# Kernel tuning notes

Measured on AMD Instinct MI355X. Metric: run time of the kernel, lower is better.

Reference implementation:

```python
import jax, jax.numpy as jnp
import numpy as np
from jax import lax

LRELU_SLOPE = 0.2
EPS = 1e-8


def eq_linear(x, W, b):
    # EqualizedLinear: weight scaled by 1/sqrt(fan_in)
    c = 1.0 / np.sqrt(W.shape[1])
    return x @ (W * c).T + b


def mod_conv(x, s, W, demod):
    # x: [b, cin, h, w], s: [b, cin], W: [cout, cin, k, k]
    b, cin, h, w = x.shape
    cout, _, k, _ = W.shape
    c = 1.0 / np.sqrt(cin * k * k)
    weights = (W * c)[None] * s[:, None, :, None, None]  # [b, cout, cin, k, k]
    if demod:
        sigma_inv = lax.rsqrt(jnp.sum(weights ** 2, axis=(2, 3, 4)) + EPS)  # [b, cout]
        weights = weights * sigma_inv[:, :, None, None, None]
    x2 = x.reshape(1, b * cin, h, w)
    wk = weights.reshape(b * cout, cin, k, k)
    pad = k // 2
    out = lax.conv_general_dilated(
        x2, wk, window_strides=(1, 1), padding=[(pad, pad), (pad, pad)],
        dimension_numbers=("NCHW", "OIHW", "NCHW"), feature_group_count=b)
    return out.reshape(b, cout, h, w)


def style_block(x, w, noise, style_W, style_b, conv_W, scale_noise, bias):
    A = eq_linear(w, style_W, style_b)          # [b, cin]
    x = mod_conv(x, A, conv_W, demod=True)      # [b, cout, h, w]
    if noise is not None:
        x = x + scale_noise[None, :, None, None] * noise
    return jax.nn.leaky_relu(x + bias[None, :, None, None], LRELU_SLOPE)


def rgb_block(x, w, style_W, style_b, conv_W, bias):
    A = eq_linear(w, style_W, style_b)
    x = mod_conv(x, A, conv_W, demod=False)     # 1x1 conv to 3 channels
    return jax.nn.leaky_relu(x + bias[None, :, None, None], LRELU_SLOPE)


def setup_inputs() -> dict:
    key = jax.random.key(0)
    ks = jax.random.split(key, 10)
    B, CIN, COUT, WD, H, W = 8, 512, 512, 512, 64, 64
    return {
        "x": jax.random.normal(ks[0], (B, CIN, H, W), jnp.float32),
        "w": jax.random.normal(ks[1], (B, WD), jnp.float32),
        "noise": jax.random.normal(ks[2], (2, B, 1, H, W), jnp.float32),
        # StyleBlock 1
        "s1_style_W": jax.random.normal(ks[3], (CIN, WD), jnp.float32),
        "s1_style_b": jnp.ones((CIN,), jnp.float32),
        "s1_conv_W": jax.random.normal(ks[4], (COUT, CIN, 3, 3), jnp.float32),
        "s1_scale_noise": jnp.zeros((1,), jnp.float32),
        "s1_bias": jnp.zeros((COUT,), jnp.float32),
        # StyleBlock 2
        "s2_style_W": jax.random.normal(ks[5], (COUT, WD), jnp.float32),
        "s2_style_b": jnp.ones((COUT,), jnp.float32),
        "s2_conv_W": jax.random.normal(ks[6], (COUT, COUT, 3, 3), jnp.float32),
        "s2_scale_noise": jnp.zeros((1,), jnp.float32),
        "s2_bias": jnp.zeros((COUT,), jnp.float32),
        # RGBBlock
        "rgb_style_W": jax.random.normal(ks[7], (COUT, WD), jnp.float32),
        "rgb_style_b": jnp.ones((COUT,), jnp.float32),
        "rgb_conv_W": jax.random.normal(ks[8], (3, COUT, 1, 1), jnp.float32),
        "rgb_bias": jnp.zeros((3,), jnp.float32),
    }


def reference(x, w, noise,
              s1_style_W, s1_style_b, s1_conv_W, s1_scale_noise, s1_bias,
              s2_style_W, s2_style_b, s2_conv_W, s2_scale_noise, s2_bias,
              rgb_style_W, rgb_style_b, rgb_conv_W, rgb_bias):
    x = style_block(x, w, noise[0], s1_style_W, s1_style_b, s1_conv_W, s1_scale_noise, s1_bias)
    x = style_block(x, w, noise[1], s2_style_W, s2_style_b, s2_conv_W, s2_scale_noise, s2_bias)
    rgb = rgb_block(x, w, rgb_style_W, rgb_style_b, rgb_conv_W, rgb_bias)
    return (x, rgb)
```

## Files before the change

kernel.cpp:

```cpp
#include <hip/hip_runtime.h>
#include <stdint.h>

typedef __attribute__((ext_vector_type(8))) short bf16x8;
typedef __attribute__((ext_vector_type(4))) float f32x4;

__device__ __forceinline__ ushort f2bf(float f) {
  uint32_t u = __builtin_bit_cast(uint32_t, f);
  u += 0x7fffu + ((u >> 16) & 1u);
  return (ushort)(u >> 16);
}

__device__ __forceinline__ void async_copy16(const void* gsrc, void* ldst) {
  __builtin_amdgcn_global_load_lds(
      (const __attribute__((address_space(1))) void*)gsrc,
      (__attribute__((address_space(3))) void*)ldst, 16, 0, 0);
}

__global__ void style_linear(const float* __restrict__ w, const float* __restrict__ sW,
                             const float* __restrict__ sb, float* __restrict__ A) {
  const int b = blockIdx.y;
  const int lane = threadIdx.x & 63, wv = threadIdx.x >> 6;
  const int co = blockIdx.x * 4 + wv;
  const float c = 0.04419417382415922f;
  const float* wr = w + b * 512;
  const float* Wr = sW + (size_t)co * 512;
  float s = 0.f;
#pragma unroll
  for (int i = 0; i < 8; ++i) {
    const int d = i * 64 + lane;
    s += wr[d] * Wr[d];
  }
#pragma unroll
  for (int off = 32; off; off >>= 1) s += __shfl_xor(s, off);
  if (lane == 0) A[b * 512 + co] = s * c + sb[co];
}

__global__ void prep_sigma(const float* __restrict__ Wc, const float* __restrict__ A,
                           ushort* __restrict__ Wt, float* __restrict__ sig) {
  const int co = blockIdx.x;
  const int ci = threadIdx.x;
  const int lane = ci & 63, wid = ci >> 6;
  const float c = 0.014731391274719738f;
  const float* src = Wc + ((size_t)co * 512 + ci) * 9;
  float s = 0.f;
#pragma unroll
  for (int t = 0; t < 9; ++t) {
    float v = src[t] * c;
    Wt[(size_t)t * 262144 + co * 512 + ci] = f2bf(v);
    s += v * v;
  }
  __shared__ float red[8][8];
#pragma unroll
  for (int b = 0; b < 8; ++b) {
    float a = A[b * 512 + ci];
    float v = s * a * a;
#pragma unroll
    for (int off = 32; off; off >>= 1) v += __shfl_xor(v, off);
    if (lane == 0) red[b][wid] = v;
  }
  __syncthreads();
  if (ci < 8) {
    float t = 0.f;
#pragma unroll
    for (int wv = 0; wv < 8; ++wv) t += red[ci][wv];
    sig[ci * 512 + co] = rsqrtf(t + 1e-8f);
  }
}

__global__ void zero_border(uint4* __restrict__ x1, uint4* __restrict__ x2) {
  const int i = blockIdx.x * 256 + threadIdx.x;
  const int per = 16640;
  const int tot = per * 8;
  if (i >= 2 * tot) return;
  uint4* base = (i < tot) ? x1 : x2;
  int t = (i < tot) ? i : i - tot;
  const int bb = t / per;
  int r = t - bb * per;
  int row, cell, q;
  if (r < 8448) {
    row = (r >= 4224) ? 65 : 0;
    int pos = (r >= 4224) ? r - 4224 : r;
    cell = pos >> 6;
    q = pos & 63;
  } else {
    int r2 = r - 8448;
    row = 1 + (r2 >> 7);
    cell = ((r2 >> 6) & 1) ? 65 : 0;
    q = r2 & 63;
  }
  base[(((size_t)bb * 66 + row) * 66 + cell) * 64 + q] = make_uint4(0u, 0u, 0u, 0u);
}

__global__ void mod_transpose(const float* __restrict__ X, const float* __restrict__ A,
                              ushort* __restrict__ xs) {
  __shared__ float tile[128][65];
  const int h = blockIdx.x;
  const int ci0 = blockIdx.y * 128;
  const int b = blockIdx.z;
  const int tid = threadIdx.x;
  const int wcol = tid & 63;
  const int r0 = tid >> 6;
#pragma unroll 4
  for (int i = 0; i < 32; ++i) {
    const int cil = r0 + i * 4;
    const int ci = ci0 + cil;
    const size_t off = ((size_t)(b * 512 + ci) * 64 + h) * 64 + wcol;
    tile[cil][wcol] = X[off] * A[b * 512 + ci];
  }
  __syncthreads();
  const int sub = tid & 3;
  const int w = tid >> 2;
  ushort* dst = xs + (((size_t)b * 66 + (h + 1)) * 66 + (w + 1)) * 512 + ci0 + sub * 32;
#pragma unroll
  for (int g = 0; g < 4; ++g) {
    bf16x8 v;
#pragma unroll
    for (int j = 0; j < 8; ++j) v[j] = (short)f2bf(tile[sub * 32 + g * 8 + j][w]);
    *(bf16x8*)(dst + g * 8) = v;
  }
}

#define WAITVM(N) asm volatile("s_waitcnt vmcnt(" #N ")" ::: "memory")

#define PHASE(S, WN, DOSTAGE)                                                        \
  do {                                                                               \
    WAITVM(WN);                                                                      \
    asm volatile("" ::: "memory");                                                   \
    __builtin_amdgcn_s_barrier();                                                    \
    asm volatile("" ::: "memory");                                                   \
    const int q_ = (S) & 3;                                                          \
    const char* baA = (const char*)(&smA[0][0] + q_ * 8192);                         \
    const char* baB = (const char*)(&smB[0][0] + q_ * 8192);                         \
    bf16x8 af[8], bv[4];                                                             \
    _Pragma("unroll") for (int m_ = 0; m_ < 8; ++m_)                                 \
        af[m_] = *(const bf16x8*)(baA + aro[m_]);                                    \
    _Pragma("unroll") for (int n_ = 0; n_ < 4; ++n_)                                 \
        bv[n_] = *(const bf16x8*)(baB + bro[n_]);                                    \
    if (DOSTAGE) stage((S) + 3);                                                     \
    __builtin_amdgcn_sched_barrier(0);                                               \
    __builtin_amdgcn_s_setprio(1);                                                   \
    _Pragma("unroll") for (int m_ = 0; m_ < 8; ++m_)                                 \
      _Pragma("unroll") for (int n_ = 0; n_ < 4; ++n_)                               \
        acc[m_][n_] = __builtin_amdgcn_mfma_f32_16x16x32_bf16(af[m_], bv[n_],        \
                                                              acc[m_][n_], 0, 0, 0); \
    __builtin_amdgcn_s_setprio(0);                                                   \
    __builtin_amdgcn_sched_barrier(0);                                               \
  } while (0)

template <int OUT_MODE>
__global__ __launch_bounds__(512, 2) void conv3x3(
    const ushort* __restrict__ xs, const ushort* __restrict__ Wt,
    const float* __restrict__ sig, const float* __restrict__ noise,
    const float* __restrict__ scale_noise, const float* __restrict__ bias,
    const float* __restrict__ amod, void* __restrict__ outp) {
  __shared__ __align__(16) ushort smA[4][8192];
  __shared__ __align__(16) ushort smB[4][8192];
  const int tid = threadIdx.x, lane = tid & 63, wid = tid >> 6;
  const int wr = wid >> 2, wc = wid & 3;
  const int id = blockIdx.x;
  const int b = id & 7;
  const int tile = id >> 3;
  const int co0 = (tile & 1) * 256;
  const int px0 = (tile >> 1) * 256;
  const int h0 = px0 >> 6;

  const int sswz = ((lane & 3) ^ ((lane >> 3) & 3)) * 8;
  int aoff[2], boff[2];
  ushort *ldsA[2], *ldsB[2];
#pragma unroll
  for (int i = 0; i < 2; ++i) {
    const int row = (i * 8 + wid) * 16 + (lane >> 2);
    aoff[i] = (co0 + row) * 512 + sswz;
    const int hh = h0 + (row >> 6), ww = row & 63;
    boff[i] = ((b * 66 + hh) * 66 + ww) * 512 + sswz;
    ldsA[i] = &smA[0][0] + (i * 8 + wid) * 512 + lane * 8;
    ldsB[i] = &smB[0][0] + (i * 8 + wid) * 512 + lane * 8;
  }
  const int rdsw = ((lane >> 4) ^ ((lane >> 1) & 3)) * 16;
  int aro[8], bro[4];
#pragma unroll
  for (int m = 0; m < 8; ++m) aro[m] = (wr * 128 + m * 16 + (lane & 15)) * 64 + rdsw;
#pragma unroll
  for (int n = 0; n < 4; ++n) bro[n] = (wc * 64 + n * 16 + (lane & 15)) * 64 + rdsw;

  f32x4 acc[8][4];
#pragma unroll
  for (int m = 0; m < 8; ++m)
#pragma unroll
    for (int n = 0; n < 4; ++n) acc[m][n] = (f32x4){0.f, 0.f, 0.f, 0.f};

  auto stage = [&](int s) {
    const int tap = s >> 4;
    const int ci0 = (s & 15) << 5;
    const int kh = tap / 3;
    const int kw = tap - kh * 3;
    const int q = s & 3;
    const ushort* Wb = Wt + tap * 262144 + ci0;
    const ushort* Xb = xs + (kh * 66 + kw) * 512 + ci0;
    async_copy16(Wb + aoff[0], ldsA[0] + q * 8192);
    async_copy16(Wb + aoff[1], ldsA[1] + q * 8192);
    async_copy16(Xb + boff[0], ldsB[0] + q * 8192);
    async_copy16(Xb + boff[1], ldsB[1] + q * 8192);
  };

  stage(0);
  stage(1);
  stage(2);

  for (int s = 0; s < 140; s += 4) {
    PHASE(s + 0, 8, true);
    PHASE(s + 1, 8, true);
    PHASE(s + 2, 8, true);
    PHASE(s + 3, 8, true);
  }
  PHASE(140, 8, true);
  PHASE(141, 8, false);
  PHASE(142, 4, false);
  PHASE(143, 0, false);

  const float sn = scale_noise[0];
  const int colp = lane & 15;
  const int rq = (lane >> 4) * 4;
  float nz[4];
#pragma unroll
  for (int n = 0; n < 4; ++n)
    nz[n] = sn * noise[b * 4096 + px0 + wc * 64 + n * 16 + colp];
#pragma unroll
  for (int m = 0; m < 8; ++m) {
    const int cob = co0 + wr * 128 + m * 16 + rq;
    float sg[4], bs[4], am[4];
#pragma unroll
    for (int r = 0; r < 4; ++r) {
      sg[r] = sig[b * 512 + cob + r];
      bs[r] = bias[cob + r];
      am[r] = (OUT_MODE == 0) ? amod[b * 512 + cob + r] : 0.f;
    }
#pragma unroll
    for (int n = 0; n < 4; ++n) {
      const int px = px0 + wc * 64 + n * 16 + colp;
      if (OUT_MODE == 0) {
        const int hh = px >> 6, ww = px & 63;
        ushort pk[4];
#pragma unroll
        for (int r = 0; r < 4; ++r) {
          float v = acc[m][n][r] * sg[r] + nz[n] + bs[r];
          v = (v > 0.f) ? v : 0.2f * v;
          pk[r] = f2bf(v * am[r]);
        }
        uint2 u;
        u.x = (uint32_t)pk[0] | ((uint32_t)pk[1] << 16);
        u.y = (uint32_t)pk[2] | ((uint32_t)pk[3] << 16);
        *(uint2*)((ushort*)outp + (((size_t)b * 66 + hh + 1) * 66 + (ww + 1)) * 512 + cob) = u;
      } else {
#pragma unroll
        for (int r = 0; r < 4; ++r) {
          float v = acc[m][n][r] * sg[r] + nz[n] + bs[r];
          v = (v > 0.f) ? v : 0.2f * v;
          ((float*)outp)[((size_t)b * 512 + cob + r) * 4096 + px] = v;
        }
      }
    }
  }
}

__global__ void rgb_k(const float* __restrict__ X, const float* __restrict__ Ar,
                      const float* __restrict__ rgbW, const float* __restrict__ rgbB,
                      float* __restrict__ out) {
  __shared__ float wmod[3 * 512];
  const int b = blockIdx.y;
  const int tid = threadIdx.x;
  const float c = 0.04419417382415922f;
  for (int idx = tid; idx < 1536; idx += 256)
    wmod[idx] = rgbW[idx] * c * Ar[b * 512 + (idx & 511)];
  __syncthreads();
  const int p = blockIdx.x * 256 + tid;
  const float* xb = X + (size_t)b * 512 * 4096 + p;
  float a0 = 0.f, a1 = 0.f, a2 = 0.f;
  for (int ci = 0; ci < 512; ++ci) {
    float xv = xb[(size_t)ci * 4096];
    a0 += wmod[ci] * xv;
    a1 += wmod[512 + ci] * xv;
    a2 += wmod[1024 + ci] * xv;
  }
  float v0 = a0 + rgbB[0], v1 = a1 + rgbB[1], v2 = a2 + rgbB[2];
  v0 = (v0 > 0.f) ? v0 : 0.2f * v0;
  v1 = (v1 > 0.f) ? v1 : 0.2f * v1;
  v2 = (v2 > 0.f) ? v2 : 0.2f * v2;
  out[((size_t)b * 3 + 0) * 4096 + p] = v0;
  out[((size_t)b * 3 + 1) * 4096 + p] = v1;
  out[((size_t)b * 3 + 2) * 4096 + p] = v2;
}

extern "C" void kernel_launch(void* const* d_in, const int* in_sizes, int n_in,
                              void* d_out, int out_size, void* d_ws, size_t ws_size,
                              hipStream_t stream) {
  const float* x     = (const float*)d_in[0];
  const float* w     = (const float*)d_in[1];
  const float* noise = (const float*)d_in[2];
  const float* s1_sW = (const float*)d_in[3];
  const float* s1_sb = (const float*)d_in[4];
  const float* s1_cW = (const float*)d_in[5];
  const float* s1_sn = (const float*)d_in[6];
  const float* s1_b  = (const float*)d_in[7];
  const float* s2_sW = (const float*)d_in[8];
  const float* s2_sb = (const float*)d_in[9];
  const float* s2_cW = (const float*)d_in[10];
  const float* s2_sn = (const float*)d_in[11];
  const float* s2_b  = (const float*)d_in[12];
  const float* r_sW  = (const float*)d_in[13];
  const float* r_sb  = (const float*)d_in[14];
  const float* r_cW  = (const float*)d_in[15];
  const float* r_b   = (const float*)d_in[16];

  char* ws = (char*)d_ws;
  float*  A1  = (float*)(ws + 0);
  float*  A2  = (float*)(ws + 16384);
  float*  Arr = (float*)(ws + 32768);
  float*  sg1 = (float*)(ws + 49152);
  float*  sg2 = (float*)(ws + 65536);
  ushort* Wt1 = (ushort*)(ws + 98304);
  ushort* xs1 = (ushort*)(ws + 4816896);
  ushort* Wt2 = (ushort*)(ws + 4816896);
  ushort* xs2 = (ushort*)(ws + 40501248);
  float* outx   = (float*)d_out;
  float* outrgb = outx + (size_t)8 * 512 * 4096;

  style_linear<<<dim3(128, 8), 256, 0, stream>>>(w, s1_sW, s1_sb, A1);
  style_linear<<<dim3(128, 8), 256, 0, stream>>>(w, s2_sW, s2_sb, A2);
  style_linear<<<dim3(128, 8), 256, 0, stream>>>(w, r_sW, r_sb, Arr);

  prep_sigma<<<512, 512, 0, stream>>>(s1_cW, A1, Wt1, sg1);

  zero_border<<<1040, 256, 0, stream>>>((uint4*)xs1, (uint4*)xs2);
  mod_transpose<<<dim3(64, 4, 8), 256, 0, stream>>>(x, A1, xs1);

  conv3x3<0><<<dim3(256), 512, 0, stream>>>(xs1, Wt1, sg1, noise, s1_sn, s1_b, A2, (void*)xs2);
  prep_sigma<<<512, 512, 0, stream>>>(s2_cW, A2, Wt2, sg2);
  conv3x3<1><<<dim3(256), 512, 0, stream>>>(xs2, Wt2, sg2, noise + 32768, s2_sn, s2_b, sg2,
                                            (void*)outx);
  rgb_k<<<dim3(16, 8), 256, 0, stream>>>(outx, Arr, r_cW, r_b, outrgb);
}
```

Baseline: 351.1 us.

## Split conv3x3 main loop into half-phases overlapping LDS reads with MFMAs

Restructures the K-loop of the conv3x3 GEMM into two sub-phases per stage. The upper half of the A fragments is read from LDS while MFMAs on the lower half run, and the next stage's lower-A and B fragments are prefetched while the upper-half MFMAs run, using double-buffered register fragments. The aim is to hide LDS read latency behind matrix-core work instead of waiting on all fragment loads before each MFMA batch. The vmcnt wait thresholds are also changed. The extra fragment registers add pressure at 512 threads with 2 blocks per CU, and the reworked barrier and wait placement risks LDS buffer races.

After: 360.5 us. +2.7%, slower.

```diff
diff --git a/kernel.cpp b/kernel.cpp
--- a/kernel.cpp
+++ b/kernel.cpp
@@ -122,29 +122,40 @@
 
 #define WAITVM(N) asm volatile("s_waitcnt vmcnt(" #N ")" ::: "memory")
 
-#define PHASE(S, WN, DOSTAGE)                                                        \
-  do {                                                                               \
-    WAITVM(WN);                                                                      \
-    asm volatile("" ::: "memory");                                                   \
-    __builtin_amdgcn_s_barrier();                                                    \
-    asm volatile("" ::: "memory");                                                   \
-    const int q_ = (S) & 3;                                                          \
-    const char* baA = (const char*)(&smA[0][0] + q_ * 8192);                         \
-    const char* baB = (const char*)(&smB[0][0] + q_ * 8192);                         \
-    bf16x8 af[8], bv[4];                                                             \
-    _Pragma("unroll") for (int m_ = 0; m_ < 8; ++m_)                                 \
-        af[m_] = *(const bf16x8*)(baA + aro[m_]);                                    \
-    _Pragma("unroll") for (int n_ = 0; n_ < 4; ++n_)                                 \
-        bv[n_] = *(const bf16x8*)(baB + bro[n_]);                                    \
-    if (DOSTAGE) stage((S) + 3);                                                     \
-    __builtin_amdgcn_sched_barrier(0);                                               \
-    __builtin_amdgcn_s_setprio(1);                                                   \
-    _Pragma("unroll") for (int m_ = 0; m_ < 8; ++m_)                                 \
-      _Pragma("unroll") for (int n_ = 0; n_ < 4; ++n_)                               \
-        acc[m_][n_] = __builtin_amdgcn_mfma_f32_16x16x32_bf16(af[m_], bv[n_],        \
-                                                              acc[m_][n_], 0, 0, 0); \
-    __builtin_amdgcn_s_setprio(0);                                                   \
-    __builtin_amdgcn_sched_barrier(0);                                               \
+#define MFMA_BF16(a, bb, c) __builtin_amdgcn_mfma_f32_16x16x32_bf16(a, bb, c, 0, 0, 0)
+
+#define SPA(S, AFL, BVC)                                                     \
+  do {                                                                       \
+    const char* baC = (const char*)(&smA[0][0]) + ((S) & 3) * 16384;         \
+    _Pragma("unroll") for (int m_ = 0; m_ < 4; ++m_)                         \
+        afH[m_] = *(const bf16x8*)(baC + aro[4 + m_]);                       \
+    __builtin_amdgcn_sched_barrier(0);                                       \
+    __builtin_amdgcn_s_setprio(1);                                           \
+    _Pragma("unroll") for (int m_ = 0; m_ < 4; ++m_)                         \
+      _Pragma("unroll") for (int n_ = 0; n_ < 4; ++n_)                       \
+          acc[m_][n_] = MFMA_BF16(AFL[m_], BVC[n_], acc[m_][n_]);            \
+    __builtin_amdgcn_s_setprio(0);                                           \
+    __builtin_amdgcn_sched_barrier(0);                                       \
+  } while (0)
+
+#define SPB(S, WN, DOSTAGE, AFLN, BVN, BVC)                                  \
+  do {                                                                       \
+    WAITVM(WN);                                                              \
+    __builtin_amdgcn_s_barrier();                                            \
+    const char* baA = (const char*)(&smA[0][0]) + (((S) + 1) & 3) * 16384;   \
+    const char* baB = (const char*)(&smB[0][0]) + (((S) + 1) & 3) * 16384;   \
+    _Pragma("unroll") for (int m_ = 0; m_ < 4; ++m_)                         \
+        AFLN[m_] = *(const bf16x8*)(baA + aro[m_]);                          \
+    _Pragma("unroll") for (int n_ = 0; n_ < 4; ++n_)                         \
+        BVN[n_] = *(const bf16x8*)(baB + bro[n_]);                           \
+    if (DOSTAGE) stage((S) + 3);                                             \
+    __builtin_amdgcn_sched_barrier(0);                                       \
+    __builtin_amdgcn_s_setprio(1);                                           \
+    _Pragma("unroll") for (int m_ = 0; m_ < 4; ++m_)                         \
+      _Pragma("unroll") for (int n_ = 0; n_ < 4; ++n_)                       \
+          acc[4 + m_][n_] = MFMA_BF16(afH[m_], BVC[n_], acc[4 + m_][n_]);    \
+    __builtin_amdgcn_s_setprio(0);                                           \
+    __builtin_amdgcn_sched_barrier(0);                                       \
   } while (0)
 
 template <int OUT_MODE>
@@ -203,20 +214,38 @@
     async_copy16(Xb + boff[1], ldsB[1] + q * 8192);
   };
 
+  bf16x8 afL0[4], afL1[4], bv0[4], bv1[4], afH[4];
+
   stage(0);
   stage(1);
   stage(2);
-
-  for (int s = 0; s < 140; s += 4) {
-    PHASE(s + 0, 8, true);
-    PHASE(s + 1, 8, true);
-    PHASE(s + 2, 8, true);
-    PHASE(s + 3, 8, true);
-  }
-  PHASE(140, 8, true);
-  PHASE(141, 8, false);
-  PHASE(142, 4, false);
-  PHASE(143, 0, false);
+  WAITVM(8);
+  __builtin_amdgcn_s_barrier();
+  {
+    const char* baA = (const char*)(&smA[0][0]);
+    const char* baB = (const char*)(&smB[0][0]);
+#pragma unroll
+    for (int m_ = 0; m_ < 4; ++m_) afL0[m_] = *(const bf16x8*)(baA + aro[m_]);
+#pragma unroll
+    for (int n_ = 0; n_ < 4; ++n_) bv0[n_] = *(const bf16x8*)(baB + bro[n_]);
+  }
+
+  for (int s = 0; s < 142; s += 2) {
+    SPA(s, afL0, bv0);
+    SPB(s, 4, (s + 3 <= 143), afL1, bv1, bv0);
+    SPA(s + 1, afL1, bv1);
+    SPB(s + 1, 4, (s + 4 <= 143), afL0, bv0, bv1);
+  }
+  SPA(142, afL0, bv0);
+  SPB(142, 0, false, afL1, bv1, bv0);
+  SPA(143, afL1, bv1);
+  __builtin_amdgcn_s_setprio(1);
+#pragma unroll
+  for (int m_ = 0; m_ < 4; ++m_)
+#pragma unroll
+    for (int n_ = 0; n_ < 4; ++n_)
+      acc[4 + m_][n_] = MFMA_BF16(afH[m_], bv1[n_], acc[4 + m_][n_]);
+  __builtin_amdgcn_s_setprio(0);
 
   const float sn = scale_noise[0];
   const int colp = lane & 15;
```

## Halve conv pixel tile and use triple-buffered LDS for higher occupancy

Applied to the files above, without the earlier changes.

The implicit-GEMM conv tile changes from 256x256 to 256 cout by 128 pixels, and each wave now computes a 64x64 sub-tile with half as many accumulators. The LDS ring drops from four stages to three, and the launch bound rises to four blocks per CU, while the grid doubles to 512 blocks. The aim is to fill all CUs and raise occupancy so latency is hidden by more resident waves. In exchange, weights are reloaded more often, data reuse per MFMA falls, and the prefetch distance is shorter.

Result: slower. 390.8 us (+11.3%).

```diff
diff --git a/kernel.cpp b/kernel.cpp
--- a/kernel.cpp
+++ b/kernel.cpp
@@ -122,24 +122,23 @@
 
 #define WAITVM(N) asm volatile("s_waitcnt vmcnt(" #N ")" ::: "memory")
 
-#define PHASE(S, WN, DOSTAGE)                                                        \
+#define PHASE(S, Q, QS, WN, DOSTAGE)                                                 \
   do {                                                                               \
     WAITVM(WN);                                                                      \
     asm volatile("" ::: "memory");                                                   \
     __builtin_amdgcn_s_barrier();                                                    \
     asm volatile("" ::: "memory");                                                   \
-    const int q_ = (S) & 3;                                                          \
-    const char* baA = (const char*)(&smA[0][0] + q_ * 8192);                         \
-    const char* baB = (const char*)(&smB[0][0] + q_ * 8192);                         \
-    bf16x8 af[8], bv[4];                                                             \
-    _Pragma("unroll") for (int m_ = 0; m_ < 8; ++m_)                                 \
+    const char* baA = (const char*)(&smA[0][0]) + (Q) * 16384;                       \
+    const char* baB = (const char*)(&smB[0][0]) + (Q) * 8192;                        \
+    bf16x8 af[4], bv[4];                                                             \
+    _Pragma("unroll") for (int m_ = 0; m_ < 4; ++m_)                                 \
         af[m_] = *(const bf16x8*)(baA + aro[m_]);                                    \
     _Pragma("unroll") for (int n_ = 0; n_ < 4; ++n_)                                 \
         bv[n_] = *(const bf16x8*)(baB + bro[n_]);                                    \
-    if (DOSTAGE) stage((S) + 3);                                                     \
+    if (DOSTAGE) stage((S) + 2, (QS));                                               \
     __builtin_amdgcn_sched_barrier(0);                                               \
     __builtin_amdgcn_s_setprio(1);                                                   \
-    _Pragma("unroll") for (int m_ = 0; m_ < 8; ++m_)                                 \
+    _Pragma("unroll") for (int m_ = 0; m_ < 4; ++m_)                                 \
       _Pragma("unroll") for (int n_ = 0; n_ < 4; ++n_)                               \
         acc[m_][n_] = __builtin_amdgcn_mfma_f32_16x16x32_bf16(af[m_], bv[n_],        \
                                                               acc[m_][n_], 0, 0, 0); \
@@ -148,75 +147,73 @@
   } while (0)
 
 template <int OUT_MODE>
-__global__ __launch_bounds__(512, 2) void conv3x3(
+__global__ __launch_bounds__(512, 4) void conv3x3(
     const ushort* __restrict__ xs, const ushort* __restrict__ Wt,
     const float* __restrict__ sig, const float* __restrict__ noise,
     const float* __restrict__ scale_noise, const float* __restrict__ bias,
     const float* __restrict__ amod, void* __restrict__ outp) {
-  __shared__ __align__(16) ushort smA[4][8192];
-  __shared__ __align__(16) ushort smB[4][8192];
-  const int tid = threadIdx.x, lane = tid & 63, wid = tid >> 6;
-  const int wr = wid >> 2, wc = wid & 3;
+  __shared__ __align__(16) ushort smA[3][8192];
+  __shared__ __align__(16) ushort smB[3][4096];
+  const int tid = threadIdx.x, lane = tid & 63;
+  const int wid = tid >> 6;
+  const int wr = wid >> 1, wc = wid & 1;
   const int id = blockIdx.x;
   const int b = id & 7;
   const int tile = id >> 3;
   const int co0 = (tile & 1) * 256;
-  const int px0 = (tile >> 1) * 256;
+  const int px0 = (tile >> 1) * 128;
   const int h0 = px0 >> 6;
 
   const int sswz = ((lane & 3) ^ ((lane >> 3) & 3)) * 8;
-  int aoff[2], boff[2];
-  ushort *ldsA[2], *ldsB[2];
-#pragma unroll
-  for (int i = 0; i < 2; ++i) {
-    const int row = (i * 8 + wid) * 16 + (lane >> 2);
-    aoff[i] = (co0 + row) * 512 + sswz;
-    const int hh = h0 + (row >> 6), ww = row & 63;
-    boff[i] = ((b * 66 + hh) * 66 + ww) * 512 + sswz;
-    ldsA[i] = &smA[0][0] + (i * 8 + wid) * 512 + lane * 8;
-    ldsB[i] = &smB[0][0] + (i * 8 + wid) * 512 + lane * 8;
-  }
+  int aoff[2], boff;
+  {
+    const int rowA0 = tid >> 2;
+    aoff[0] = (co0 + rowA0) * 512 + sswz;
+    aoff[1] = (co0 + 128 + rowA0) * 512 + sswz;
+    const int rowB = tid >> 2;
+    const int hh = h0 + (rowB >> 6), ww = rowB & 63;
+    boff = ((b * 66 + hh) * 66 + ww) * 512 + sswz;
+  }
+  ushort* ldsA0 = &smA[0][0] + tid * 8;
+  ushort* ldsA1 = &smA[0][0] + 4096 + tid * 8;
+  ushort* ldsB0 = &smB[0][0] + tid * 8;
+
   const int rdsw = ((lane >> 4) ^ ((lane >> 1) & 3)) * 16;
-  int aro[8], bro[4];
-#pragma unroll
-  for (int m = 0; m < 8; ++m) aro[m] = (wr * 128 + m * 16 + (lane & 15)) * 64 + rdsw;
+  int aro[4], bro[4];
+#pragma unroll
+  for (int m = 0; m < 4; ++m) aro[m] = (wr * 64 + m * 16 + (lane & 15)) * 64 + rdsw;
 #pragma unroll
   for (int n = 0; n < 4; ++n) bro[n] = (wc * 64 + n * 16 + (lane & 15)) * 64 + rdsw;
 
-  f32x4 acc[8][4];
-#pragma unroll
-  for (int m = 0; m < 8; ++m)
+  f32x4 acc[4][4];
+#pragma unroll
+  for (int m = 0; m < 4; ++m)
 #pragma unroll
     for (int n = 0; n < 4; ++n) acc[m][n] = (f32x4){0.f, 0.f, 0.f, 0.f};
 
-  auto stage = [&](int s) {
+  auto stage = [&](int s, int q) {
     const int tap = s >> 4;
     const int ci0 = (s & 15) << 5;
     const int kh = tap / 3;
     const int kw = tap - kh * 3;
-    const int q = s & 3;
     const ushort* Wb = Wt + tap * 262144 + ci0;
     const ushort* Xb = xs + (kh * 66 + kw) * 512 + ci0;
-    async_copy16(Wb + aoff[0], ldsA[0] + q * 8192);
-    async_copy16(Wb + aoff[1], ldsA[1] + q * 8192);
-    async_copy16(Xb + boff[0], ldsB[0] + q * 8192);
-    async_copy16(Xb + boff[1], ldsB[1] + q * 8192);
+    async_copy16(Wb + aoff[0], ldsA0 + q * 8192);
+    async_copy16(Wb + aoff[1], ldsA1 + q * 8192);
+    async_copy16(Xb + boff, ldsB0 + q * 4096);
   };
 
-  stage(0);
-  stage(1);
-  stage(2);
-
-  for (int s = 0; s < 140; s += 4) {
-    PHASE(s + 0, 8, true);
-    PHASE(s + 1, 8, true);
-    PHASE(s + 2, 8, true);
-    PHASE(s + 3, 8, true);
-  }
-  PHASE(140, 8, true);
-  PHASE(141, 8, false);
-  PHASE(142, 4, false);
-  PHASE(143, 0, false);
+  stage(0, 0);
+  stage(1, 1);
+
+  for (int s = 0; s < 141; s += 3) {
+    PHASE(s + 0, 0, 2, 3, true);
+    PHASE(s + 1, 1, 0, 3, true);
+    PHASE(s + 2, 2, 1, 3, true);
+  }
+  PHASE(141, 0, 2, 3, true);
+  PHASE(142, 1, 0, 3, false);
+  PHASE(143, 2, 1, 0, false);
 
   const float sn = scale_noise[0];
   const int colp = lane & 15;
@@ -226,8 +223,8 @@
   for (int n = 0; n < 4; ++n)
     nz[n] = sn * noise[b * 4096 + px0 + wc * 64 + n * 16 + colp];
 #pragma unroll
-  for (int m = 0; m < 8; ++m) {
-    const int cob = co0 + wr * 128 + m * 16 + rq;
+  for (int m = 0; m < 4; ++m) {
+    const int cob = co0 + wr * 64 + m * 16 + rq;
     float sg[4], bs[4], am[4];
 #pragma unroll
     for (int r = 0; r < 4; ++r) {
@@ -334,9 +331,9 @@
   zero_border<<<1040, 256, 0, stream>>>((uint4*)xs1, (uint4*)xs2);
   mod_transpose<<<dim3(64, 4, 8), 256, 0, stream>>>(x, A1, xs1);
 
-  conv3x3<0><<<dim3(256), 512, 0, stream>>>(xs1, Wt1, sg1, noise, s1_sn, s1_b, A2, (void*)xs2);
+  conv3x3<0><<<dim3(512), 512, 0, stream>>>(xs1, Wt1, sg1, noise, s1_sn, s1_b, A2, (void*)xs2);
   prep_sigma<<<512, 512, 0, stream>>>(s2_cW, A2, Wt2, sg2);
-  conv3x3<1><<<dim3(256), 512, 0, stream>>>(xs2, Wt2, sg2, noise + 32768, s2_sn, s2_b, sg2,
+  conv3x3<1><<<dim3(512), 512, 0, stream>>>(xs2, Wt2, sg2, noise + 32768, s2_sn, s2_b, sg2,
                                             (void*)outx);
   rgb_k<<<dim3(16, 8), 256, 0, stream>>>(outx, Arr, r_cW, r_b, outrgb);
 }
```
